# Performance work log

Measured on AMD Instinct MI355X. Metric: run time of the kernel, lower is better.

The kernel has to match this reference:

```python
import jax, jax.numpy as jnp
import numpy as np

N, S, L, E, H = 8, 2, 512, 1024, 16
D = E // H  # head_dim = 64


def setup_inputs() -> dict:
    key = jax.random.key(0)
    ks = jax.random.split(key, 10)
    inp = {
        "values": jax.random.normal(ks[0], (N, S, L, E), dtype=jnp.float32),
        "keys": jax.random.normal(ks[1], (N, S, L, E), dtype=jnp.float32),
        "query": jax.random.normal(ks[2], (N, S, L, E), dtype=jnp.float32),
        "mask": jax.random.randint(ks[3], (N, S, L, 1), 0, 2, dtype=jnp.int32),
        # per-head projection weights, nn.Linear(D, D, bias=False): y = x @ W.T
        "Wv": jax.random.normal(ks[4], (D, D), dtype=jnp.float32) / np.sqrt(D),
        "Wk": jax.random.normal(ks[5], (D, D), dtype=jnp.float32) / np.sqrt(D),
        "Wq": jax.random.normal(ks[6], (D, D), dtype=jnp.float32) / np.sqrt(D),
        # output projection nn.Linear(E, E)
        "Wo": jax.random.normal(ks[7], (E, E), dtype=jnp.float32) / np.sqrt(E),
        "bo": jax.random.normal(ks[8], (E,), dtype=jnp.float32) * 0.01,
    }
    return inp


def reference(values, keys, query, mask, Wv, Wk, Wq, Wo, bo):
    n, s, l, e = query.shape
    h, d = H, D
    key_len = keys.shape[2]
    # split heads: (n, s, len, h, d)
    v = values.reshape(n, s, l, h, d) @ Wv.T
    k = keys.reshape(n, s, l, h, d) @ Wk.T
    q = query.reshape(n, s, l, h, d) @ Wq.T
    # energy: (n, s, h, q_len, k_len)
    energy = jnp.einsum('nsqhd,nskhd->nshqk', q, k)
    # mask[:, :, :, 0] masks QUERY positions (broadcast over heads and k)
    m = mask[:, :, :, 0]  # (n, s, l)
    energy = jnp.where(m[:, :, None, :, None] == 0, jnp.float32(-1e20), energy)
    # NOTE: softmax over the QUERY axis (dim=3), faithful to the original
    attn = jax.nn.softmax(energy / jnp.sqrt(jnp.float32(key_len)), axis=3)
    out = jnp.einsum('nshql,nslhd->nsqhd', attn, v)
    out = out.reshape(n, s, l, h * d)
    return out @ Wo.T + bo
```

## Files before the change

kernel.cpp:

```cpp
#include <hip/hip_runtime.h>
#include <math.h>

#define LL 512
#define EE 1024
#define HH 16
#define DD 64
#define NSX 16
#define NT (NSX*LL)
#define NSLE (NT*EE)
#define SCALE_Q 0.06375871f

typedef unsigned short u16;
typedef short bf16x8 __attribute__((ext_vector_type(8)));
typedef float f32x4 __attribute__((ext_vector_type(4)));

__device__ inline u16 f2bf(float f) {
  unsigned u = __float_as_uint(f);
  u += 0x7fff + ((u >> 16) & 1);
  return (u16)(u >> 16);
}

#define FEXP2(x) __builtin_amdgcn_exp2f(x)
#define MFMA32(a, b, c) __builtin_amdgcn_mfma_f32_16x16x32_bf16((a), (b), (c), 0, 0, 0)

__global__ void __launch_bounds__(256) convw_kernel(
    const float* __restrict__ Wv, const float* __restrict__ Wk,
    const float* __restrict__ Wq, const float* __restrict__ Wo,
    u16* __restrict__ Wvb, u16* __restrict__ Wkb,
    u16* __restrict__ Wqb, u16* __restrict__ Wob) {
  int i = blockIdx.x * 256 + threadIdx.x;
  const float* s; u16* d; int j;
  if (i < 262144) { s = Wo; d = Wob; j = i; }
  else {
    j = i - 262144;
    if (j < 1024)      { s = Wv; d = Wvb; }
    else if (j < 2048) { s = Wk; d = Wkb; j -= 1024; }
    else               { s = Wq; d = Wqb; j -= 2048; }
  }
  float4 f = ((const float4*)s)[j];
  ushort4 o; o.x = f2bf(f.x); o.y = f2bf(f.y); o.z = f2bf(f.z); o.w = f2bf(f.w);
  ((ushort4*)d)[j] = o;
}

__global__ void __launch_bounds__(256) proj_kernel(
    const float* __restrict__ vals, const float* __restrict__ keys,
    const float* __restrict__ qry,
    const u16* __restrict__ Wvb, const u16* __restrict__ Wkb,
    const u16* __restrict__ Wqb,
    u16* __restrict__ vpT, u16* __restrict__ kp, u16* __restrict__ qp) {
  const int b = blockIdx.x;
  const int tt0 = b & 7, hg = (b >> 3) & 3, ns = (b >> 5) & 15, mat = b >> 9;
  const int tid = threadIdx.x;
  const int wid = tid >> 6, lane = tid & 63, quad = lane >> 4, l16 = lane & 15;
  const int h = hg*4 + wid;
  const float* src = (mat == 0 ? vals : mat == 1 ? keys : qry);
  const u16*   W   = (mat == 0 ? Wvb  : mat == 1 ? Wkb  : Wqb);
  u16* dst = (mat == 1 ? kp : qp);
  const float sc = (mat == 2) ? SCALE_Q : 1.f;
  bf16x8 wf[4][2];
  #pragma unroll
  for (int nt = 0; nt < 4; ++nt) {
    wf[nt][0] = *(const bf16x8*)&W[(nt*16 + l16)*DD + quad*8];
    wf[nt][1] = *(const bf16x8*)&W[(nt*16 + l16)*DD + 32 + quad*8];
  }
  f32x4 z = {0.f, 0.f, 0.f, 0.f};
  const float* xrow0 = src + (size_t)(ns*LL + tt0*16 + l16)*EE + h*DD;
  float4 x0 = *(const float4*)&xrow0[quad*8];
  float4 x1 = *(const float4*)&xrow0[quad*8 + 4];
  float4 x2 = *(const float4*)&xrow0[32 + quad*8];
  float4 x3 = *(const float4*)&xrow0[32 + quad*8 + 4];
  #pragma unroll
  for (int j = 0; j < 4; ++j) {
    const int tt = tt0 + 8*j;
    const int t0 = ns*LL + tt*16;
    float4 n0, n1, n2, n3;
    if (j < 3) {
      const float* xrown = src + (size_t)(t0 + 8*16 + l16)*EE + h*DD;
      n0 = *(const float4*)&xrown[quad*8];
      n1 = *(const float4*)&xrown[quad*8 + 4];
      n2 = *(const float4*)&xrown[32 + quad*8];
      n3 = *(const float4*)&xrown[32 + quad*8 + 4];
    }
    bf16x8 af0, af1;
    af0[0] = (short)f2bf(x0.x); af0[1] = (short)f2bf(x0.y);
    af0[2] = (short)f2bf(x0.z); af0[3] = (short)f2bf(x0.w);
    af0[4] = (short)f2bf(x1.x); af0[5] = (short)f2bf(x1.y);
    af0[6] = (short)f2bf(x1.z); af0[7] = (short)f2bf(x1.w);
    af1[0] = (short)f2bf(x2.x); af1[1] = (short)f2bf(x2.y);
    af1[2] = (short)f2bf(x2.z); af1[3] = (short)f2bf(x2.w);
    af1[4] = (short)f2bf(x3.x); af1[5] = (short)f2bf(x3.y);
    af1[6] = (short)f2bf(x3.z); af1[7] = (short)f2bf(x3.w);
    f32x4 acc[4];
    #pragma unroll
    for (int nt = 0; nt < 4; ++nt) {
      acc[nt] = MFMA32(af0, wf[nt][0], z);
      acc[nt] = MFMA32(af1, wf[nt][1], acc[nt]);
    }
    if (mat == 0) {
      #pragma unroll
      for (int nt = 0; nt < 4; ++nt) {
        ushort4 o;
        o.x = f2bf(acc[nt][0]); o.y = f2bf(acc[nt][1]);
        o.z = f2bf(acc[nt][2]); o.w = f2bf(acc[nt][3]);
        size_t idx = ((size_t)((ns*HH + h)*DD + nt*16 + l16))*LL + tt*16 + quad*4;
        *(ushort4*)&vpT[idx] = o;
      }
    } else {
      #pragma unroll
      for (int nt = 0; nt < 4; ++nt)
        #pragma unroll
        for (int r = 0; r < 4; ++r)
          dst[(size_t)(t0 + quad*4 + r)*EE + h*DD + nt*16 + l16] =
              f2bf(acc[nt][r] * sc);
    }
    x0 = n0; x1 = n1; x2 = n2; x3 = n3;
  }
}

__global__ void __launch_bounds__(1024, 4) attn_kernel(
    const u16* __restrict__ qp, const u16* __restrict__ kp,
    const u16* __restrict__ vpT, const int* __restrict__ mask,
    u16* __restrict__ oat) {
  const int b = blockIdx.x;
  const int h = b & 15, ns = b >> 4;
  const int tid = threadIdx.x;
  const int wid = tid >> 6, lane = tid & 63, quad = lane >> 4, l16 = lane & 15;
  __shared__ u16 Ks[LL][72];
  __shared__ u16 Vt[2][DD][72];
  __shared__ u16 pt[16][32][40];
  __shared__ float csum[LL];
  float* psum = (float*)pt;
  const size_t kgbase = ((size_t)(ns*LL))*EE + h*DD;
  for (int i = tid; i < 4096; i += 1024) {
    int row = i >> 3, seg = (i & 7) * 8;
    *(bf16x8*)&Ks[row][seg] = *(const bf16x8*)&kp[kgbase + (size_t)row*EE + seg];
  }
  const int q0 = wid*32;
  bf16x8 qf[2][2];
  float maf[2][4];
  #pragma unroll
  for (int qt = 0; qt < 2; ++qt) {
    const u16* qrow = qp + ((size_t)(ns*LL + q0 + qt*16 + l16))*EE + h*DD;
    qf[qt][0] = *(const bf16x8*)&qrow[quad*8];
    qf[qt][1] = *(const bf16x8*)&qrow[32 + quad*8];
    #pragma unroll
    for (int r = 0; r < 4; ++r)
      maf[qt][r] = mask[ns*LL + q0 + qt*16 + quad*4 + r] ? 1.f : 0.f;
  }
  f32x4 z = {0.f, 0.f, 0.f, 0.f};
  __syncthreads();
  for (int lt = 0; lt < 32; ++lt) {
    bf16x8 kf0 = *(const bf16x8*)&Ks[lt*16 + l16][quad*8];
    bf16x8 kf1 = *(const bf16x8*)&Ks[lt*16 + l16][32 + quad*8];
    float part = 0.f;
    #pragma unroll
    for (int qt = 0; qt < 2; ++qt) {
      f32x4 e = MFMA32(qf[qt][0], kf0, z);
      e = MFMA32(qf[qt][1], kf1, e);
      #pragma unroll
      for (int r = 0; r < 4; ++r)
        part += maf[qt][r] * FEXP2(e[r]);
    }
    part += __shfl_xor(part, 16);
    part += __shfl_xor(part, 32);
    if (quad == 0) psum[wid*512 + lt*16 + l16] = part;
  }
  __syncthreads();
  if (tid < LL) {
    float s = 0.f;
    #pragma unroll
    for (int w = 0; w < 16; ++w) s += psum[w*512 + tid];
    csum[tid] = (s > 0.f) ? 1.f/s : 0.f;
  }
  __syncthreads();
  f32x4 acc[4][2] = {{z,z},{z,z},{z,z},{z,z}};
  const size_t vgbase = ((size_t)((ns*HH + h)*DD))*LL;
  for (int lc = 0; lc < 8; ++lc) {
    if (tid < 512) {
      int row = tid >> 3, seg = (tid & 7) * 8;
      *(bf16x8*)&Vt[lc & 1][row][seg] =
          *(const bf16x8*)&vpT[vgbase + (size_t)row*LL + lc*64 + seg];
    }
    __syncthreads();
    #pragma unroll
    for (int lt2 = 0; lt2 < 4; ++lt2) {
      const int lrow = lc*64 + lt2*16 + l16;
      bf16x8 kf0 = *(const bf16x8*)&Ks[lrow][quad*8];
      bf16x8 kf1 = *(const bf16x8*)&Ks[lrow][32 + quad*8];
      const float csv = csum[lrow];
      #pragma unroll
      for (int qt = 0; qt < 2; ++qt) {
        f32x4 e = MFMA32(qf[qt][0], kf0, z);
        e = MFMA32(qf[qt][1], kf1, e);
        #pragma unroll
        for (int r = 0; r < 4; ++r)
          pt[wid][qt*16 + quad*4 + r][lt2 & 1 ? 16 + l16 : l16] =
              f2bf(maf[qt][r] * csv * FEXP2(e[r]));
        if (lt2 & 1) {
          bf16x8 pa = *(const bf16x8*)&pt[wid][qt*16 + l16][quad*8];
          #pragma unroll
          for (int dt = 0; dt < 4; ++dt) {
            bf16x8 vb = *(const bf16x8*)&Vt[lc & 1][dt*16 + l16]
                                        [(lt2 >> 1)*32 + quad*8];
            acc[dt][qt] = MFMA32(pa, vb, acc[dt][qt]);
          }
        }
      }
    }
  }
  #pragma unroll
  for (int qt = 0; qt < 2; ++qt)
    #pragma unroll
    for (int dt = 0; dt < 4; ++dt)
      #pragma unroll
      for (int r = 0; r < 4; ++r)
        oat[((size_t)(ns*LL + q0 + qt*16 + quad*4 + r))*EE + h*DD + dt*16 + l16] =
            f2bf(acc[dt][qt][r]);
}

__global__ void __launch_bounds__(256) out_gemm_kernel(
    const u16* __restrict__ A, const u16* __restrict__ Wob,
    const float* __restrict__ bo, float* __restrict__ Y) {
  __shared__ u16 As[128][72];
  __shared__ u16 Bs[128][72];
  const int b = blockIdx.x;
  const int nb = b & 7, mb = b >> 3;
  const int m0 = mb*128, n0 = nb*128;
  const int tid = threadIdx.x;
  const int wid = tid >> 6, lane = tid & 63, quad = lane >> 4, l16 = lane & 15;
  const int wm = (wid >> 1)*64, wn = (wid & 1)*64;
  f32x4 z = {0.f, 0.f, 0.f, 0.f};
  f32x4 acc[4][4];
  #pragma unroll
  for (int i = 0; i < 4; ++i)
    #pragma unroll
    for (int j = 0; j < 4; ++j) acc[i][j] = z;
  for (int k0 = 0; k0 < EE; k0 += 64) {
    __syncthreads();
    #pragma unroll
    for (int it = 0; it < 4; ++it) {
      int idx = it*256 + tid;
      int row = idx >> 3, seg = (idx & 7) * 8;
      *(bf16x8*)&As[row][seg] = *(const bf16x8*)&A  [(size_t)(m0 + row)*EE + k0 + seg];
      *(bf16x8*)&Bs[row][seg] = *(const bf16x8*)&Wob[(size_t)(n0 + row)*EE + k0 + seg];
    }
    __syncthreads();
    #pragma unroll
    for (int kk = 0; kk < 2; ++kk) {
      bf16x8 af[4], bfr[4];
      #pragma unroll
      for (int i = 0; i < 4; ++i)
        af[i] = *(const bf16x8*)&As[wm + i*16 + l16][kk*32 + quad*8];
      #pragma unroll
      for (int j = 0; j < 4; ++j)
        bfr[j] = *(const bf16x8*)&Bs[wn + j*16 + l16][kk*32 + quad*8];
      #pragma unroll
      for (int i = 0; i < 4; ++i)
        #pragma unroll
        for (int j = 0; j < 4; ++j)
          acc[i][j] = MFMA32(af[i], bfr[j], acc[i][j]);
    }
  }
  #pragma unroll
  for (int i = 0; i < 4; ++i)
    #pragma unroll
    for (int j = 0; j < 4; ++j) {
      int col = n0 + wn + j*16 + l16;
      float bias = bo[col];
      #pragma unroll
      for (int r = 0; r < 4; ++r)
        Y[(size_t)(m0 + wm + i*16 + quad*4 + r)*EE + col] = acc[i][j][r] + bias;
    }
}

extern "C" void kernel_launch(void* const* d_in, const int* in_sizes, int n_in,
                              void* d_out, int out_size, void* d_ws, size_t ws_size,
                              hipStream_t stream) {
  const float* values = (const float*)d_in[0];
  const float* keysp  = (const float*)d_in[1];
  const float* query  = (const float*)d_in[2];
  const int*   mask   = (const int*)d_in[3];
  const float* Wv = (const float*)d_in[4];
  const float* Wk = (const float*)d_in[5];
  const float* Wq = (const float*)d_in[6];
  const float* Wo = (const float*)d_in[7];
  const float* bo = (const float*)d_in[8];
  float* Y = (float*)d_out;

  u16* qp  = (u16*)d_ws;
  u16* kp  = qp + NSLE;
  u16* vpT = kp + NSLE;
  u16* oat = vpT + NSLE;
  u16* Wob = oat + NSLE;
  u16* Wvb = Wob + EE*EE;
  u16* Wkb = Wvb + DD*DD;
  u16* Wqb = Wkb + DD*DD;

  convw_kernel<<<1036, 256, 0, stream>>>(Wv, Wk, Wq, Wo, Wvb, Wkb, Wqb, Wob);
  proj_kernel<<<3*NSX*4*8, 256, 0, stream>>>(values, keysp, query,
                                             Wvb, Wkb, Wqb, vpT, kp, qp);
  attn_kernel<<<NSX*HH, 1024, 0, stream>>>(qp, kp, vpT, mask, oat);
  out_gemm_kernel<<<(NT/128)*(EE/128), 256, 0, stream>>>(oat, Wob, bo, Y);
}
```

Measured before the change: 227.9 us.

## Keep P in registers, use direct-to-LDS loads, double projection grid

The attention kernel now computes the transposed score tile (K as the A operand). It rebuilds the P operand for the PV MFMA with cross-lane shuffles instead of a round trip through shared memory, and writes the output with vectorized stores. The output GEMM now stages A and W tiles with global_load_lds direct-to-LDS loads and unpadded shared arrays, which may add bank conflicts on the fragment reads. The projection kernel launches twice as many blocks, each doing two row tiles instead of four, to raise parallelism.

```diff
diff --git a/kernel.cpp b/kernel.cpp
--- a/kernel.cpp
+++ b/kernel.cpp
@@ -11,6 +11,7 @@
 #define SCALE_Q 0.06375871f
 
 typedef unsigned short u16;
+typedef unsigned int u32t;
 typedef short bf16x8 __attribute__((ext_vector_type(8)));
 typedef float f32x4 __attribute__((ext_vector_type(4)));
 
@@ -22,6 +23,12 @@
 
 #define FEXP2(x) __builtin_amdgcn_exp2f(x)
 #define MFMA32(a, b, c) __builtin_amdgcn_mfma_f32_16x16x32_bf16((a), (b), (c), 0, 0, 0)
+
+__device__ inline void gload16(const void* g, void* l) {
+  __builtin_amdgcn_global_load_lds(
+      (const __attribute__((address_space(1))) unsigned int*)g,
+      (__attribute__((address_space(3))) unsigned int*)l, 16, 0, 0);
+}
 
 __global__ void __launch_bounds__(256) convw_kernel(
     const float* __restrict__ Wv, const float* __restrict__ Wk,
@@ -49,7 +56,7 @@
     const u16* __restrict__ Wqb,
     u16* __restrict__ vpT, u16* __restrict__ kp, u16* __restrict__ qp) {
   const int b = blockIdx.x;
-  const int tt0 = b & 7, hg = (b >> 3) & 3, ns = (b >> 5) & 15, mat = b >> 9;
+  const int tt0 = b & 15, hg = (b >> 4) & 3, ns = (b >> 6) & 15, mat = b >> 10;
   const int tid = threadIdx.x;
   const int wid = tid >> 6, lane = tid & 63, quad = lane >> 4, l16 = lane & 15;
   const int h = hg*4 + wid;
@@ -70,12 +77,12 @@
   float4 x2 = *(const float4*)&xrow0[32 + quad*8];
   float4 x3 = *(const float4*)&xrow0[32 + quad*8 + 4];
   #pragma unroll
-  for (int j = 0; j < 4; ++j) {
-    const int tt = tt0 + 8*j;
+  for (int j = 0; j < 2; ++j) {
+    const int tt = tt0 + 16*j;
     const int t0 = ns*LL + tt*16;
     float4 n0, n1, n2, n3;
-    if (j < 3) {
-      const float* xrown = src + (size_t)(t0 + 8*16 + l16)*EE + h*DD;
+    if (j < 1) {
+      const float* xrown = src + (size_t)(t0 + 256 + l16)*EE + h*DD;
       n0 = *(const float4*)&xrown[quad*8];
       n1 = *(const float4*)&xrown[quad*8 + 4];
       n2 = *(const float4*)&xrown[32 + quad*8];
@@ -127,9 +134,8 @@
   const int wid = tid >> 6, lane = tid & 63, quad = lane >> 4, l16 = lane & 15;
   __shared__ u16 Ks[LL][72];
   __shared__ u16 Vt[2][DD][72];
-  __shared__ u16 pt[16][32][40];
+  __shared__ float psum[16][512];
   __shared__ float csum[LL];
-  float* psum = (float*)pt;
   const size_t kgbase = ((size_t)(ns*LL))*EE + h*DD;
   for (int i = tid; i < 4096; i += 1024) {
     int row = i >> 3, seg = (i & 7) * 8;
@@ -138,6 +144,7 @@
   const int q0 = wid*32;
   bf16x8 qf[2][2];
   float maf[2][4];
+  float mqf[2];
   #pragma unroll
   for (int qt = 0; qt < 2; ++qt) {
     const u16* qrow = qp + ((size_t)(ns*LL + q0 + qt*16 + l16))*EE + h*DD;
@@ -146,6 +153,7 @@
     #pragma unroll
     for (int r = 0; r < 4; ++r)
       maf[qt][r] = mask[ns*LL + q0 + qt*16 + quad*4 + r] ? 1.f : 0.f;
+    mqf[qt] = mask[ns*LL + q0 + qt*16 + l16] ? 1.f : 0.f;
   }
   f32x4 z = {0.f, 0.f, 0.f, 0.f};
   __syncthreads();
@@ -163,13 +171,13 @@
     }
     part += __shfl_xor(part, 16);
     part += __shfl_xor(part, 32);
-    if (quad == 0) psum[wid*512 + lt*16 + l16] = part;
+    if (quad == 0) psum[wid][lt*16 + l16] = part;
   }
   __syncthreads();
   if (tid < LL) {
     float s = 0.f;
     #pragma unroll
-    for (int w = 0; w < 16; ++w) s += psum[w*512 + tid];
+    for (int w = 0; w < 16; ++w) s += psum[w][tid];
     csum[tid] = (s > 0.f) ? 1.f/s : 0.f;
   }
   __syncthreads();
@@ -183,52 +191,83 @@
     }
     __syncthreads();
     #pragma unroll
-    for (int lt2 = 0; lt2 < 4; ++lt2) {
-      const int lrow = lc*64 + lt2*16 + l16;
-      bf16x8 kf0 = *(const bf16x8*)&Ks[lrow][quad*8];
-      bf16x8 kf1 = *(const bf16x8*)&Ks[lrow][32 + quad*8];
-      const float csv = csum[lrow];
-      #pragma unroll
-      for (int qt = 0; qt < 2; ++qt) {
-        f32x4 e = MFMA32(qf[qt][0], kf0, z);
-        e = MFMA32(qf[qt][1], kf1, e);
+    for (int hf = 0; hf < 2; ++hf) {
+      const int lb = lc*64 + hf*32;
+      u32t pu[2][2][2];
+      #pragma unroll
+      for (int t = 0; t < 2; ++t) {
+        const int lrow = lb + t*16 + l16;
+        bf16x8 kf0 = *(const bf16x8*)&Ks[lrow][quad*8];
+        bf16x8 kf1 = *(const bf16x8*)&Ks[lrow][32 + quad*8];
+        float4 cs4 = *(const float4*)&csum[lb + t*16 + quad*4];
         #pragma unroll
-        for (int r = 0; r < 4; ++r)
-          pt[wid][qt*16 + quad*4 + r][lt2 & 1 ? 16 + l16 : l16] =
-              f2bf(maf[qt][r] * csv * FEXP2(e[r]));
-        if (lt2 & 1) {
-          bf16x8 pa = *(const bf16x8*)&pt[wid][qt*16 + l16][quad*8];
-          #pragma unroll
-          for (int dt = 0; dt < 4; ++dt) {
-            bf16x8 vb = *(const bf16x8*)&Vt[lc & 1][dt*16 + l16]
-                                        [(lt2 >> 1)*32 + quad*8];
-            acc[dt][qt] = MFMA32(pa, vb, acc[dt][qt]);
-          }
+        for (int qt = 0; qt < 2; ++qt) {
+          f32x4 e = MFMA32(kf0, qf[qt][0], z);
+          e = MFMA32(kf1, qf[qt][1], e);
+          const float m = mqf[qt];
+          u32t p0 = f2bf(FEXP2(e[0]) * (cs4.x * m));
+          u32t p1 = f2bf(FEXP2(e[1]) * (cs4.y * m));
+          u32t p2 = f2bf(FEXP2(e[2]) * (cs4.z * m));
+          u32t p3 = f2bf(FEXP2(e[3]) * (cs4.w * m));
+          pu[qt][t][0] = p0 | (p1 << 16);
+          pu[qt][t][1] = p2 | (p3 << 16);
         }
       }
-    }
-  }
-  #pragma unroll
-  for (int qt = 0; qt < 2; ++qt)
-    #pragma unroll
-    for (int dt = 0; dt < 4; ++dt)
-      #pragma unroll
-      for (int r = 0; r < 4; ++r)
-        oat[((size_t)(ns*LL + q0 + qt*16 + quad*4 + r))*EE + h*DD + dt*16 + l16] =
-            f2bf(acc[dt][qt][r]);
+      bf16x8 vb[4];
+      #pragma unroll
+      for (int dt = 0; dt < 4; ++dt)
+        vb[dt] = *(const bf16x8*)&Vt[lc & 1][dt*16 + l16][hf*32 + quad*8];
+      const int srcLo = (quad & 1)*32 + l16;
+      const int srcHi = srcLo + 16;
+      const bool hiq = quad >= 2;
+      #pragma unroll
+      for (int qt = 0; qt < 2; ++qt) {
+        u32t a0 = (u32t)__shfl((int)pu[qt][0][0], srcLo);
+        u32t a1 = (u32t)__shfl((int)pu[qt][0][1], srcLo);
+        u32t a2 = (u32t)__shfl((int)pu[qt][0][0], srcHi);
+        u32t a3 = (u32t)__shfl((int)pu[qt][0][1], srcHi);
+        u32t b0 = (u32t)__shfl((int)pu[qt][1][0], srcLo);
+        u32t b1 = (u32t)__shfl((int)pu[qt][1][1], srcLo);
+        u32t b2 = (u32t)__shfl((int)pu[qt][1][0], srcHi);
+        u32t b3 = (u32t)__shfl((int)pu[qt][1][1], srcHi);
+        union { u32t u[4]; bf16x8 v; } pb;
+        pb.u[0] = hiq ? b0 : a0;
+        pb.u[1] = hiq ? b1 : a1;
+        pb.u[2] = hiq ? b2 : a2;
+        pb.u[3] = hiq ? b3 : a3;
+        #pragma unroll
+        for (int dt = 0; dt < 4; ++dt)
+          acc[dt][qt] = MFMA32(vb[dt], pb.v, acc[dt][qt]);
+      }
+    }
+  }
+  #pragma unroll
+  for (int qt = 0; qt < 2; ++qt) {
+    const size_t obase = ((size_t)(ns*LL + q0 + qt*16 + l16))*EE + h*DD;
+    #pragma unroll
+    for (int dt = 0; dt < 4; ++dt) {
+      ushort4 o;
+      o.x = f2bf(acc[dt][qt][0]); o.y = f2bf(acc[dt][qt][1]);
+      o.z = f2bf(acc[dt][qt][2]); o.w = f2bf(acc[dt][qt][3]);
+      *(ushort4*)&oat[obase + dt*16 + quad*4] = o;
+    }
+  }
 }
 
 __global__ void __launch_bounds__(256) out_gemm_kernel(
     const u16* __restrict__ A, const u16* __restrict__ Wob,
     const float* __restrict__ bo, float* __restrict__ Y) {
-  __shared__ u16 As[128][72];
-  __shared__ u16 Bs[128][72];
+  __shared__ u16 As[128][64];
+  __shared__ u16 Bs[128][64];
   const int b = blockIdx.x;
   const int nb = b & 7, mb = b >> 3;
   const int m0 = mb*128, n0 = nb*128;
   const int tid = threadIdx.x;
   const int wid = tid >> 6, lane = tid & 63, quad = lane >> 4, l16 = lane & 15;
   const int wm = (wid >> 1)*64, wn = (wid & 1)*64;
+  const int r0 = tid >> 3, sseg = (tid & 7) * 8;
+  u16* adst = &As[0][0] + tid*8;
+  u16* bdst = &Bs[0][0] + tid*8;
   f32x4 z = {0.f, 0.f, 0.f, 0.f};
   f32x4 acc[4][4];
   #pragma unroll
@@ -239,10 +278,8 @@
     __syncthreads();
     #pragma unroll
     for (int it = 0; it < 4; ++it) {
-      int idx = it*256 + tid;
-      int row = idx >> 3, seg = (idx & 7) * 8;
-      *(bf16x8*)&As[row][seg] = *(const bf16x8*)&A  [(size_t)(m0 + row)*EE + k0 + seg];
-      *(bf16x8*)&Bs[row][seg] = *(const bf16x8*)&Wob[(size_t)(n0 + row)*EE + k0 + seg];
+      gload16(&A  [(size_t)(m0 + it*32 + r0)*EE + k0 + sseg], adst + it*2048);
+      gload16(&Wob[(size_t)(n0 + it*32 + r0)*EE + k0 + sseg], bdst + it*2048);
     }
     __syncthreads();
     #pragma unroll
@@ -297,8 +334,8 @@
   u16* Wqb = Wkb + DD*DD;
 
   convw_kernel<<<1036, 256, 0, stream>>>(Wv, Wk, Wq, Wo, Wvb, Wkb, Wqb, Wob);
-  proj_kernel<<<3*NSX*4*8, 256, 0, stream>>>(values, keysp, query,
-                                             Wvb, Wkb, Wqb, vpT, kp, qp);
+  proj_kernel<<<3*NSX*4*16, 256, 0, stream>>>(values, keysp, query,
+                                              Wvb, Wkb, Wqb, vpT, kp, qp);
   attn_kernel<<<NSX*HH, 1024, 0, stream>>>(qp, kp, vpT, mask, oat);
   out_gemm_kernel<<<(NT/128)*(EE/128), 256, 0, stream>>>(oat, Wob, bo, Y);
 }
```

New measurement: 240.1 us. +5.4%, slower.

## Deepen projection prefetch, transpose Q/K MFMA stores, add setprio and direct LDS loads

Applied to the files above, without the earlier changes.

The projection kernel now prefetches two row tiles ahead. For Q and K it swaps the MFMA operands so each lane writes contiguous ushort4 stores instead of scattered scalar u16 stores. The attention kernel wraps its MFMA sequences in s_setprio to favour matrix issue across waves. The output GEMM replaces register-staged global-to-LDS copies with global_load_lds direct loads into unpadded tiles, which may add LDS bank conflicts on the fragment reads and needs a wait before the barrier to be safe.

```diff
diff --git a/kernel.cpp b/kernel.cpp
--- a/kernel.cpp
+++ b/kernel.cpp
@@ -22,6 +22,12 @@
 
 #define FEXP2(x) __builtin_amdgcn_exp2f(x)
 #define MFMA32(a, b, c) __builtin_amdgcn_mfma_f32_16x16x32_bf16((a), (b), (c), 0, 0, 0)
+
+__device__ inline void gload16(const void* g, void* l) {
+  __builtin_amdgcn_global_load_lds(
+      (const __attribute__((address_space(1))) unsigned int*)g,
+      (__attribute__((address_space(3))) unsigned int*)l, 16, 0, 0);
+}
 
 __global__ void __launch_bounds__(256) convw_kernel(
     const float* __restrict__ Wv, const float* __restrict__ Wk,
@@ -64,22 +70,27 @@
     wf[nt][1] = *(const bf16x8*)&W[(nt*16 + l16)*DD + 32 + quad*8];
   }
   f32x4 z = {0.f, 0.f, 0.f, 0.f};
-  const float* xrow0 = src + (size_t)(ns*LL + tt0*16 + l16)*EE + h*DD;
-  float4 x0 = *(const float4*)&xrow0[quad*8];
-  float4 x1 = *(const float4*)&xrow0[quad*8 + 4];
-  float4 x2 = *(const float4*)&xrow0[32 + quad*8];
-  float4 x3 = *(const float4*)&xrow0[32 + quad*8 + 4];
+  const float* xr0 = src + (size_t)(ns*LL + tt0*16 + l16)*EE + h*DD;
+  const float* xr1 = xr0 + (size_t)128*EE;
+  float4 x0 = *(const float4*)&xr0[quad*8];
+  float4 x1 = *(const float4*)&xr0[quad*8 + 4];
+  float4 x2 = *(const float4*)&xr0[32 + quad*8];
+  float4 x3 = *(const float4*)&xr0[32 + quad*8 + 4];
+  float4 y0 = *(const float4*)&xr1[quad*8];
+  float4 y1 = *(const float4*)&xr1[quad*8 + 4];
+  float4 y2 = *(const float4*)&xr1[32 + quad*8];
+  float4 y3 = *(const float4*)&xr1[32 + quad*8 + 4];
   #pragma unroll
   for (int j = 0; j < 4; ++j) {
     const int tt = tt0 + 8*j;
     const int t0 = ns*LL + tt*16;
     float4 n0, n1, n2, n3;
-    if (j < 3) {
-      const float* xrown = src + (size_t)(t0 + 8*16 + l16)*EE + h*DD;
-      n0 = *(const float4*)&xrown[quad*8];
-      n1 = *(const float4*)&xrown[quad*8 + 4];
-      n2 = *(const float4*)&xrown[32 + quad*8];
-      n3 = *(const float4*)&xrown[32 + quad*8 + 4];
+    if (j < 2) {
+      const float* xrn = src + (size_t)(t0 + 256 + l16)*EE + h*DD;
+      n0 = *(const float4*)&xrn[quad*8];
+      n1 = *(const float4*)&xrn[quad*8 + 4];
+      n2 = *(const float4*)&xrn[32 + quad*8];
+      n3 = *(const float4*)&xrn[32 + quad*8 + 4];
     }
     bf16x8 af0, af1;
     af0[0] = (short)f2bf(x0.x); af0[1] = (short)f2bf(x0.y);
@@ -90,13 +101,13 @@
     af1[2] = (short)f2bf(x2.z); af1[3] = (short)f2bf(x2.w);
     af1[4] = (short)f2bf(x3.x); af1[5] = (short)f2bf(x3.y);
     af1[6] = (short)f2bf(x3.z); af1[7] = (short)f2bf(x3.w);
-    f32x4 acc[4];
-    #pragma unroll
-    for (int nt = 0; nt < 4; ++nt) {
-      acc[nt] = MFMA32(af0, wf[nt][0], z);
-      acc[nt] = MFMA32(af1, wf[nt][1], acc[nt]);
-    }
     if (mat == 0) {
+      f32x4 acc[4];
+      #pragma unroll
+      for (int nt = 0; nt < 4; ++nt) {
+        acc[nt] = MFMA32(af0, wf[nt][0], z);
+        acc[nt] = MFMA32(af1, wf[nt][1], acc[nt]);
+      }
       #pragma unroll
       for (int nt = 0; nt < 4; ++nt) {
         ushort4 o;
@@ -106,14 +117,22 @@
         *(ushort4*)&vpT[idx] = o;
       }
     } else {
-      #pragma unroll
-      for (int nt = 0; nt < 4; ++nt)
-        #pragma unroll
-        for (int r = 0; r < 4; ++r)
-          dst[(size_t)(t0 + quad*4 + r)*EE + h*DD + nt*16 + l16] =
-              f2bf(acc[nt][r] * sc);
-    }
-    x0 = n0; x1 = n1; x2 = n2; x3 = n3;
+      f32x4 acc[4];
+      #pragma unroll
+      for (int nt = 0; nt < 4; ++nt) {
+        acc[nt] = MFMA32(wf[nt][0], af0, z);
+        acc[nt] = MFMA32(wf[nt][1], af1, acc[nt]);
+      }
+      #pragma unroll
+      for (int nt = 0; nt < 4; ++nt) {
+        ushort4 o;
+        o.x = f2bf(acc[nt][0] * sc); o.y = f2bf(acc[nt][1] * sc);
+        o.z = f2bf(acc[nt][2] * sc); o.w = f2bf(acc[nt][3] * sc);
+        *(ushort4*)&dst[(size_t)(t0 + l16)*EE + h*DD + nt*16 + quad*4] = o;
+      }
+    }
+    x0 = y0; x1 = y1; x2 = y2; x3 = y3;
+    if (j < 2) { y0 = n0; y1 = n1; y2 = n2; y3 = n3; }
   }
 }
 
@@ -155,8 +174,10 @@
     float part = 0.f;
     #pragma unroll
     for (int qt = 0; qt < 2; ++qt) {
+      __builtin_amdgcn_s_setprio(1);
       f32x4 e = MFMA32(qf[qt][0], kf0, z);
       e = MFMA32(qf[qt][1], kf1, e);
+      __builtin_amdgcn_s_setprio(0);
       #pragma unroll
       for (int r = 0; r < 4; ++r)
         part += maf[qt][r] * FEXP2(e[r]);
@@ -190,20 +211,24 @@
       const float csv = csum[lrow];
       #pragma unroll
       for (int qt = 0; qt < 2; ++qt) {
+        __builtin_amdgcn_s_setprio(1);
         f32x4 e = MFMA32(qf[qt][0], kf0, z);
         e = MFMA32(qf[qt][1], kf1, e);
+        __builtin_amdgcn_s_setprio(0);
         #pragma unroll
         for (int r = 0; r < 4; ++r)
           pt[wid][qt*16 + quad*4 + r][lt2 & 1 ? 16 + l16 : l16] =
               f2bf(maf[qt][r] * csv * FEXP2(e[r]));
         if (lt2 & 1) {
           bf16x8 pa = *(const bf16x8*)&pt[wid][qt*16 + l16][quad*8];
+          __builtin_amdgcn_s_setprio(1);
           #pragma unroll
           for (int dt = 0; dt < 4; ++dt) {
             bf16x8 vb = *(const bf16x8*)&Vt[lc & 1][dt*16 + l16]
                                         [(lt2 >> 1)*32 + quad*8];
             acc[dt][qt] = MFMA32(pa, vb, acc[dt][qt]);
           }
+          __builtin_amdgcn_s_setprio(0);
         }
       }
     }
@@ -221,14 +246,17 @@
 __global__ void __launch_bounds__(256) out_gemm_kernel(
     const u16* __restrict__ A, const u16* __restrict__ Wob,
     const float* __restrict__ bo, float* __restrict__ Y) {
-  __shared__ u16 As[128][72];
-  __shared__ u16 Bs[128][72];
+  __shared__ u16 As[128][64];
+  __shared__ u16 Bs[128][64];
   const int b = blockIdx.x;
   const int nb = b & 7, mb = b >> 3;
   const int m0 = mb*128, n0 = nb*128;
   const int tid = threadIdx.x;
   const int wid = tid >> 6, lane = tid & 63, quad = lane >> 4, l16 = lane & 15;
   const int wm = (wid >> 1)*64, wn = (wid & 1)*64;
+  const int r0 = tid >> 3, sseg = (tid & 7) * 8;
+  u16* adst = &As[0][0] + tid*8;
+  u16* bdst = &Bs[0][0] + tid*8;
   f32x4 z = {0.f, 0.f, 0.f, 0.f};
   f32x4 acc[4][4];
   #pragma unroll
@@ -239,10 +267,8 @@
     __syncthreads();
     #pragma unroll
     for (int it = 0; it < 4; ++it) {
-      int idx = it*256 + tid;
-      int row = idx >> 3, seg = (idx & 7) * 8;
-      *(bf16x8*)&As[row][seg] = *(const bf16x8*)&A  [(size_t)(m0 + row)*EE + k0 + seg];
-      *(bf16x8*)&Bs[row][seg] = *(const bf16x8*)&Wob[(size_t)(n0 + row)*EE + k0 + seg];
+      gload16(&A  [(size_t)(m0 + it*32 + r0)*EE + k0 + sseg], adst + it*2048);
+      gload16(&Wob[(size_t)(n0 + it*32 + r0)*EE + k0 + sseg], bdst + it*2048);
     }
     __syncthreads();
     #pragma unroll
```

Measured after the change: 232.8 us. 1.02x slower.
